# Kernel tuning notes

Measured on AMD Instinct MI355X. Metric: run time of the kernel, lower is better.

The kernel has to match this reference:

```python
import jax, jax.numpy as jnp
import numpy as np

BN_EPS = 1e-5

def _conv1x1(w, b, x):
    # w: (O, C), b: (O,), x: (B, C, T) -> (B, O, T)
    return jnp.einsum('oc,bct->bot', w, x) + b[None, :, None]

def _maxpool2(x):
    # MaxPool1d(kernel_size=2, stride=2): (B, C, T) -> (B, C, T//2)
    B, C, T = x.shape
    return x.reshape(B, C, T // 2, 2).max(axis=-1)

def setup_inputs() -> dict:
    key = jax.random.key(0)
    ks = jax.random.split(key, 11)
    B, C, Ci, T = 4, 256, 128, 8192
    s_in = 1.0 / np.sqrt(C)
    s_ic = 1.0 / np.sqrt(Ci)
    return {
        'x':       jax.random.normal(ks[0], (B, C, T), dtype=jnp.float32),
        'theta_w': jax.random.uniform(ks[1], (Ci, C), jnp.float32, -s_in, s_in),
        'theta_b': jax.random.uniform(ks[2], (Ci,),   jnp.float32, -s_in, s_in),
        'phi_w':   jax.random.uniform(ks[3], (Ci, C), jnp.float32, -s_in, s_in),
        'phi_b':   jax.random.uniform(ks[4], (Ci,),   jnp.float32, -s_in, s_in),
        'g_w':     jax.random.uniform(ks[5], (Ci, C), jnp.float32, -s_in, s_in),
        'g_b':     jax.random.uniform(ks[6], (Ci,),   jnp.float32, -s_in, s_in),
        'w_w':     jax.random.uniform(ks[7], (C, Ci), jnp.float32, -s_ic, s_ic),
        'w_b':     jax.random.uniform(ks[8], (C,),    jnp.float32, -s_ic, s_ic),
        'gamma':   jax.random.normal(ks[9], (C,), dtype=jnp.float32),
        'beta':    jax.random.normal(ks[10], (C,), dtype=jnp.float32),
    }

def reference(x, theta_w, theta_b, phi_w, phi_b, g_w, g_b, w_w, w_b, gamma, beta):
    # x: (B, C, T)
    theta = _conv1x1(theta_w, theta_b, x)            # (B, Ci, T)
    phi   = _maxpool2(_conv1x1(phi_w, phi_b, x))     # (B, Ci, N), N = T//2
    g     = _maxpool2(_conv1x1(g_w, g_b, x))         # (B, Ci, N)
    N = phi.shape[-1]
    # f = theta^T phi / N  (dot-product similarity, divide-by-N normalization)
    f = jnp.einsum('bct,bcn->btn', theta, phi) / N   # (B, T, N)
    y = jnp.einsum('btn,bcn->bct', f, g)             # (B, Ci, T)
    wy = _conv1x1(w_w, w_b, y)                       # (B, C, T)
    # BatchNorm1d (training mode: batch statistics over (B, T), biased var)
    mean = wy.mean(axis=(0, 2), keepdims=True)
    var = ((wy - mean) ** 2).mean(axis=(0, 2), keepdims=True)
    bn = gamma[None, :, None] * (wy - mean) * jax.lax.rsqrt(var + BN_EPS) + beta[None, :, None]
    return bn + x
```

## Files before the change

kernel.cpp:

```cpp
#include <hip/hip_runtime.h>
#include <hip/hip_bf16.h>


constexpr int B = 4, C = 256, CI = 128, T = 8192, NN = 4096;
constexpr int KP = 768, BK = 32, NSTEP = KP / BK;

using s16x8 = __attribute__((ext_vector_type(8))) short;
using f32x4 = __attribute__((ext_vector_type(4))) float;

__device__ __forceinline__ unsigned short f2bf(float f) {
    unsigned int x = __float_as_uint(f);
    unsigned int r = (x + 0x7fffu + ((x >> 16) & 1u)) >> 16;
    return (unsigned short)r;
}
__device__ __forceinline__ float bf2f(unsigned short u) {
    return __uint_as_float((unsigned int)u << 16);
}

#define MFMA(a, b, c) __builtin_amdgcn_mfma_f32_16x16x32_bf16((a), (b), (c), 0, 0, 0)

__device__ __forceinline__ void glds16(const unsigned short* g, void* l) {
    __builtin_amdgcn_global_load_lds(
        (const __attribute__((address_space(1))) unsigned int*)(g),
        (__attribute__((address_space(3))) unsigned int*)(l), 16, 0, 0);
}

constexpr size_t SZ_XT = (size_t)B * T * C * 2;
constexpr size_t O_XTH = 0;
constexpr size_t O_XTL = O_XTH + SZ_XT;
constexpr size_t O_WSH = O_XTL + SZ_XT;
constexpr size_t O_WSL = O_WSH + (size_t)C * C * 2;
constexpr size_t SZ_P  = (size_t)B * CI * NN * 2;
constexpr size_t O_PH  = O_WSL + (size_t)C * C * 2;
constexpr size_t O_PL  = O_PH + SZ_P;
constexpr size_t O_GH  = O_PL + SZ_P;
constexpr size_t O_GL  = O_GH + SZ_P;
constexpr size_t O_S   = O_GL + SZ_P;
constexpr size_t O_M   = O_S  + (size_t)B * CI * CI * 4;
constexpr size_t O_W2H = O_M  + (size_t)B * C * CI * 4;
constexpr size_t O_W2L = O_W2H + (size_t)B * C * C * 2;
constexpr size_t O_B2  = O_W2L + (size_t)B * C * C * 2;
constexpr size_t O_GS  = O_B2 + (size_t)B * C * 4;
constexpr size_t O_GQ  = O_GS + (size_t)C * 4;
constexpr size_t O_A   = O_GQ + (size_t)C * 4;
constexpr size_t O_SH  = O_A  + (size_t)C * 4;

__global__ __launch_bounds__(256) void k0_split(
    const float* __restrict__ x, unsigned short* __restrict__ xth,
    unsigned short* __restrict__ xtl)
{
    __shared__ float xs[64][65];
    int t0 = blockIdx.x * 64, c0 = blockIdx.y * 64, b = blockIdx.z;
    int tid = threadIdx.x;
    const float* xb = x + (size_t)b * C * T;
    #pragma unroll
    for (int p = 0; p < 4; ++p) {
        int idx = tid + p * 256;
        int cr = idx >> 4;
        int tg = (idx & 15) * 4;
        float4 v = *reinterpret_cast<const float4*>(xb + (size_t)(c0 + cr) * T + t0 + tg);
        xs[tg + 0][cr] = v.x; xs[tg + 1][cr] = v.y;
        xs[tg + 2][cr] = v.z; xs[tg + 3][cr] = v.w;
    }
    __syncthreads();
    #pragma unroll
    for (int p = 0; p < 2; ++p) {
        int idx = tid + p * 256;
        int cg = idx & 7, tl = idx >> 3;
        s16x8 hs, ls;
        #pragma unroll
        for (int j = 0; j < 8; ++j) {
            float v = xs[tl][cg * 8 + j];
            unsigned short h = f2bf(v);
            unsigned short l = f2bf(v - bf2f(h));
            hs[j] = (short)h; ls[j] = (short)l;
        }
        size_t dst = ((size_t)b * T + t0 + tl) * C + c0 + cg * 8;
        *reinterpret_cast<s16x8*>(xth + dst) = hs;
        *reinterpret_cast<s16x8*>(xtl + dst) = ls;
    }
}

__global__ __launch_bounds__(256) void k0w(
    const float* __restrict__ phi_w, const float* __restrict__ g_w,
    unsigned short* __restrict__ wsh, unsigned short* __restrict__ wsl)
{
    int idx = blockIdx.x * 256 + threadIdx.x;
    int row = idx >> 8, c = idx & 255;
    float v = (row < CI) ? phi_w[(size_t)row * C + c] : g_w[(size_t)(row - CI) * C + c];
    unsigned short h = f2bf(v);
    wsh[idx] = h;
    wsl[idx] = f2bf(v - bf2f(h));
}

#define STAGE_(buf, kk) {                                                      \
    const int r_ = (kk) >> 8, cb_ = (kk) & 255;                                \
    const unsigned short* As_ = (r_ == 1) ? aSrcL : aSrcH;                     \
    const unsigned short* Bs_ = (r_ == 2) ? bSrcL : bSrcH;                     \
    const unsigned short* ga_ = As_ + (size_t)lane * C + cb_ + w * 8;          \
    const unsigned short* gb_ = Bs_ + (size_t)lane * C + cb_ + w * 8;          \
    char* la_ = arena + ((buf) * 8 + w) * 2048;                                \
    char* lb_ = arena + ((buf) * 8 + 4 + w) * 2048;                            \
    glds16(ga_, la_);                                                          \
    glds16(ga_ + 64 * C, la_ + 1024);                                          \
    glds16(gb_, lb_);                                                          \
    glds16(gb_ + 64 * C, lb_ + 1024);                                          \
}

#define GEMM_LOOP() {                                                          \
    STAGE_(0, 0);                                                              \
    __syncthreads();                                                           \
    int cur = 0;                                                               \
    for (int ks = 0; ks < NSTEP; ++ks) {                                       \
        if (ks + 1 < NSTEP) { STAGE_(cur ^ 1, (ks + 1) * BK); }                \
        s16x8 af[4], bf[4];                                                    \
        _Pragma("unroll")                                                      \
        for (int ts = 0; ts < 4; ++ts)                                         \
            af[ts] = *(const s16x8*)(arena + (cur * 8 + lk) * 2048             \
                                     + (wt * 64 + ts * 16 + lr) * 16);         \
        _Pragma("unroll")                                                      \
        for (int os = 0; os < 4; ++os)                                         \
            bf[os] = *(const s16x8*)(arena + (cur * 8 + 4 + lk) * 2048         \
                                     + (wo * 64 + os * 16 + lr) * 16);         \
        _Pragma("unroll")                                                      \
        for (int os = 0; os < 4; ++os)                                         \
            _Pragma("unroll")                                                  \
            for (int ts = 0; ts < 4; ++ts)                                     \
                acc[os][ts] = MFMA(af[ts], bf[os], acc[os][ts]);               \
        __syncthreads();                                                       \
        cur ^= 1;                                                              \
    }                                                                          \
}

__global__ __launch_bounds__(256) void k1_mfma(
    const unsigned short* __restrict__ xth, const unsigned short* __restrict__ xtl,
    const unsigned short* __restrict__ wsh, const unsigned short* __restrict__ wsl,
    const float* __restrict__ phi_b, const float* __restrict__ g_b,
    unsigned short* __restrict__ ph, unsigned short* __restrict__ pl,
    unsigned short* __restrict__ gh, unsigned short* __restrict__ gl)
{
    const int b = blockIdx.z, t0 = blockIdx.x * 128, isG = blockIdx.y;
    __shared__ __align__(16) char arena[33280];
    const int tid = threadIdx.x, lane = tid & 63, w = tid >> 6;
    const int lr = lane & 15, lk = lane >> 4;
    const int wt = w >> 1, wo = w & 1;

    const unsigned short* aSrcH = xth + (size_t)(b * T + t0) * C;
    const unsigned short* aSrcL = xtl + (size_t)(b * T + t0) * C;
    const unsigned short* bSrcH = wsh + (size_t)(isG * CI) * C;
    const unsigned short* bSrcL = wsl + (size_t)(isG * CI) * C;

    f32x4 acc[4][4];
    #pragma unroll
    for (int i = 0; i < 4; ++i)
        #pragma unroll
        for (int j = 0; j < 4; ++j) acc[i][j] = (f32x4){0.f, 0.f, 0.f, 0.f};

    GEMM_LOOP()

    unsigned int (*pool_s)[65] = (unsigned int (*)[65])arena;
    const float* biasArr = isG ? g_b : phi_b;
    #pragma unroll
    for (int os = 0; os < 4; ++os) {
        int oL = wo * 64 + os * 16 + lr;
        float bias = biasArr[oL];
        #pragma unroll
        for (int ts = 0; ts < 4; ++ts) {
            f32x4 v = acc[os][ts];
            float m0 = fmaxf(v[0], v[1]) + bias;
            float m1 = fmaxf(v[2], v[3]) + bias;
            int nl = wt * 32 + ts * 8 + lk * 2;
            unsigned short h0 = f2bf(m0), h1 = f2bf(m1);
            pool_s[oL][nl]     = (unsigned int)h0 | ((unsigned int)f2bf(m0 - bf2f(h0)) << 16);
            pool_s[oL][nl + 1] = (unsigned int)h1 | ((unsigned int)f2bf(m1 - bf2f(h1)) << 16);
        }
    }
    __syncthreads();
    int oL = tid >> 1, seg = tid & 1;
    size_t n0 = (size_t)(t0 >> 1) + seg * 32;
    unsigned short* dh = (isG ? gh : ph) + ((size_t)b * CI + oL) * NN + n0;
    unsigned short* dl = (isG ? gl : pl) + ((size_t)b * CI + oL) * NN + n0;
    #pragma unroll
    for (int g4 = 0; g4 < 4; ++g4) {
        s16x8 hs, ls;
        #pragma unroll
        for (int j = 0; j < 8; ++j) {
            unsigned int u = pool_s[oL][seg * 32 + g4 * 8 + j];
            hs[j] = (short)(u & 0xffffu);
            ls[j] = (short)(u >> 16);
        }
        *reinterpret_cast<s16x8*>(dh + g4 * 8) = hs;
        *reinterpret_cast<s16x8*>(dl + g4 * 8) = ls;
    }
}

template <int MODE>
__global__ __launch_bounds__(256) void k45_mfma(
    const unsigned short* __restrict__ xth, const unsigned short* __restrict__ xtl,
    const unsigned short* __restrict__ w2h, const unsigned short* __restrict__ w2l,
    const float* __restrict__ b2, const float* __restrict__ x,
    const float* __restrict__ abuf, const float* __restrict__ shbuf,
    float* __restrict__ gsum, float* __restrict__ gsq, float* __restrict__ out)
{
    const int b = blockIdx.z, t0 = blockIdx.x * 128, o0 = blockIdx.y * 128;
    __shared__ __align__(16) char arena[32768];
    const int tid = threadIdx.x, lane = tid & 63, w = tid >> 6;
    const int lr = lane & 15, lk = lane >> 4;
    const int wt = w >> 1, wo = w & 1;

    const unsigned short* aSrcH = xth + (size_t)(b * T + t0) * C;
    const unsigned short* aSrcL = xtl + (size_t)(b * T + t0) * C;
    const unsigned short* bSrcH = w2h + ((size_t)b * C + o0) * C;
    const unsigned short* bSrcL = w2l + ((size_t)b * C + o0) * C;

    f32x4 acc[4][4];
    #pragma unroll
    for (int i = 0; i < 4; ++i)
        #pragma unroll
        for (int j = 0; j < 4; ++j) acc[i][j] = (f32x4){0.f, 0.f, 0.f, 0.f};

    GEMM_LOOP()

    #pragma unroll
    for (int os = 0; os < 4; ++os) {
        int o = o0 + wo * 64 + os * 16 + lr;
        float bv = b2[(size_t)b * C + o];
        if (MODE == 0) {
            float s = 0.f, q = 0.f;
            #pragma unroll
            for (int ts = 0; ts < 4; ++ts)
                #pragma unroll
                for (int r = 0; r < 4; ++r) {
                    float v = acc[os][ts][r] + bv;
                    s += v; q += v * v;
                }
            s += __shfl_xor(s, 16); s += __shfl_xor(s, 32);
            q += __shfl_xor(q, 16); q += __shfl_xor(q, 32);
            if (lk == 0) { atomicAdd(&gsum[o], s); atomicAdd(&gsq[o], q); }
        } else {
            float av = abuf[o], sv = shbuf[o];
            #pragma unroll
            for (int ts = 0; ts < 4; ++ts) {
                int t = t0 + wt * 64 + ts * 16 + lk * 4;
                size_t base = ((size_t)b * C + o) * T + t;
                float4 xv = *reinterpret_cast<const float4*>(x + base);
                float4 ov;
                ov.x = av * (acc[os][ts][0] + bv) + sv + xv.x;
                ov.y = av * (acc[os][ts][1] + bv) + sv + xv.y;
                ov.z = av * (acc[os][ts][2] + bv) + sv + xv.z;
                ov.w = av * (acc[os][ts][3] + bv) + sv + xv.w;
                *reinterpret_cast<float4*>(out + base) = ov;
            }
        }
    }
}

__global__ __launch_bounds__(256) void k2_mfma(
    const unsigned short* __restrict__ ph, const unsigned short* __restrict__ pl,
    const unsigned short* __restrict__ gh, const unsigned short* __restrict__ gl,
    float* __restrict__ S)
{
    int b = blockIdx.y, n0 = blockIdx.x * 128;
    int tid = threadIdx.x, lane = tid & 63, w = tid >> 6;
    int lr = lane & 15, lk = lane >> 4;

    f32x4 acc[2][8];
    #pragma unroll
    for (int i = 0; i < 2; ++i)
        #pragma unroll
        for (int j = 0; j < 8; ++j) acc[i][j] = (f32x4){0.f, 0.f, 0.f, 0.f};

    const unsigned short* ah_b = gh + ((size_t)b * CI + w * 32 + lr) * NN + n0 + lk * 8;
    const unsigned short* al_b = gl + ((size_t)b * CI + w * 32 + lr) * NN + n0 + lk * 8;
    const unsigned short* bh_b = ph + ((size_t)b * CI + lr) * NN + n0 + lk * 8;
    const unsigned short* bl_b = pl + ((size_t)b * CI + lr) * NN + n0 + lk * 8;

    for (int ks = 0; ks < 4; ++ks) {
        s16x8 Ah[2], Al[2], Bh[8], Bl[8];
        #pragma unroll
        for (int is = 0; is < 2; ++is) {
            Ah[is] = *reinterpret_cast<const s16x8*>(ah_b + (size_t)is * 16 * NN + ks * 32);
            Al[is] = *reinterpret_cast<const s16x8*>(al_b + (size_t)is * 16 * NN + ks * 32);
        }
        #pragma unroll
        for (int js = 0; js < 8; ++js) {
            Bh[js] = *reinterpret_cast<const s16x8*>(bh_b + (size_t)js * 16 * NN + ks * 32);
            Bl[js] = *reinterpret_cast<const s16x8*>(bl_b + (size_t)js * 16 * NN + ks * 32);
        }
        #pragma unroll
        for (int is = 0; is < 2; ++is)
            #pragma unroll
            for (int js = 0; js < 8; ++js) {
                acc[is][js] = MFMA(Ah[is], Bh[js], acc[is][js]);
                acc[is][js] = MFMA(Al[is], Bh[js], acc[is][js]);
                acc[is][js] = MFMA(Ah[is], Bl[js], acc[is][js]);
            }
    }
    #pragma unroll
    for (int is = 0; is < 2; ++is) {
        int i0 = w * 32 + is * 16 + lk * 4;
        #pragma unroll
        for (int js = 0; js < 8; ++js) {
            int j = js * 16 + lr;
            #pragma unroll
            for (int r = 0; r < 4; ++r)
                atomicAdd(&S[((size_t)b * CI + i0 + r) * CI + j], acc[is][js][r]);
        }
    }
}

__global__ __launch_bounds__(256) void k3a_M(
    const float* __restrict__ w_w, const float* __restrict__ S, float* __restrict__ M)
{
    int idx = blockIdx.x * 256 + threadIdx.x;
    int j4 = (idx & 31) * 4;
    int r  = (idx >> 5) & (C - 1);
    int b  = idx >> 13;
    const float* Sb = S + (size_t)b * CI * CI;
    const float* wr = w_w + (size_t)r * CI;
    float4 a = {0.f, 0.f, 0.f, 0.f};
    for (int k = 0; k < CI; ++k) {
        float wv = wr[k];
        float4 s = *reinterpret_cast<const float4*>(&Sb[(size_t)k * CI + j4]);
        a.x += wv * s.x; a.y += wv * s.y; a.z += wv * s.z; a.w += wv * s.w;
    }
    const float sc = 1.f / NN;
    a.x *= sc; a.y *= sc; a.z *= sc; a.w *= sc;
    *reinterpret_cast<float4*>(&M[((size_t)b * C + r) * CI + j4]) = a;
}

__global__ __launch_bounds__(256) void k3b_W2(
    const float* __restrict__ M, const float* __restrict__ theta_w,
    const float* __restrict__ theta_b, const float* __restrict__ w_b,
    unsigned short* __restrict__ w2h, unsigned short* __restrict__ w2l,
    float* __restrict__ b2)
{
    int idx = blockIdx.x * 256 + threadIdx.x;
    int c4 = (idx & 63) * 4;
    int r  = (idx >> 6) & (C - 1);
    int b  = idx >> 14;
    const float* Mb = M + ((size_t)b * C + r) * CI;
    float4 a = {0.f, 0.f, 0.f, 0.f};
    for (int k = 0; k < CI; ++k) {
        float mv = Mb[k];
        float4 tw = *reinterpret_cast<const float4*>(&theta_w[(size_t)k * C + c4]);
        a.x += mv * tw.x; a.y += mv * tw.y; a.z += mv * tw.z; a.w += mv * tw.w;
    }
    size_t ob = ((size_t)b * C + r) * C + c4;
    float av[4] = {a.x, a.y, a.z, a.w};
    #pragma unroll
    for (int i = 0; i < 4; ++i) {
        unsigned short h = f2bf(av[i]);
        w2h[ob + i] = h;
        w2l[ob + i] = f2bf(av[i] - bf2f(h));
    }
    if (c4 == 0) {
        float bv = 0.f;
        for (int k = 0; k < CI; ++k) bv += Mb[k] * theta_b[k];
        b2[(size_t)b * C + r] = bv + w_b[r];
    }
}

__global__ void k4b_stats(const float* __restrict__ gsum, const float* __restrict__ gsq,
                          const float* __restrict__ gamma, const float* __restrict__ beta,
                          float* __restrict__ a, float* __restrict__ sh)
{
    int c = threadIdx.x;
    const float invBT = 1.f / (float)(B * T);
    float mean = gsum[c] * invBT;
    float var  = gsq[c] * invBT - mean * mean;
    float av = gamma[c] * rsqrtf(var + 1e-5f);
    a[c]  = av;
    sh[c] = beta[c] - av * mean;
}

extern "C" void kernel_launch(void* const* d_in, const int* in_sizes, int n_in,
                              void* d_out, int out_size, void* d_ws, size_t ws_size,
                              hipStream_t stream)
{
    const float* x       = (const float*)d_in[0];
    const float* theta_w = (const float*)d_in[1];
    const float* theta_b = (const float*)d_in[2];
    const float* phi_w   = (const float*)d_in[3];
    const float* phi_b   = (const float*)d_in[4];
    const float* g_w     = (const float*)d_in[5];
    const float* g_b     = (const float*)d_in[6];
    const float* w_w     = (const float*)d_in[7];
    const float* w_b     = (const float*)d_in[8];
    const float* gamma   = (const float*)d_in[9];
    const float* beta    = (const float*)d_in[10];
    float* out = (float*)d_out;
    char* ws = (char*)d_ws;

    unsigned short* xth = (unsigned short*)(ws + O_XTH);
    unsigned short* xtl = (unsigned short*)(ws + O_XTL);
    unsigned short* wsh = (unsigned short*)(ws + O_WSH);
    unsigned short* wsl = (unsigned short*)(ws + O_WSL);
    unsigned short* ph  = (unsigned short*)(ws + O_PH);
    unsigned short* pl  = (unsigned short*)(ws + O_PL);
    unsigned short* gh  = (unsigned short*)(ws + O_GH);
    unsigned short* gl  = (unsigned short*)(ws + O_GL);
    float* Sbuf  = (float*)(ws + O_S);
    float* Mbuf  = (float*)(ws + O_M);
    unsigned short* w2h = (unsigned short*)(ws + O_W2H);
    unsigned short* w2l = (unsigned short*)(ws + O_W2L);
    float* b2    = (float*)(ws + O_B2);
    float* gsum  = (float*)(ws + O_GS);
    float* gsq   = (float*)(ws + O_GQ);
    float* abuf  = (float*)(ws + O_A);
    float* shbuf = (float*)(ws + O_SH);

    hipMemsetAsync(Sbuf, 0, (size_t)B * CI * CI * sizeof(float), stream);
    hipMemsetAsync(gsum, 0, 2 * (size_t)C * sizeof(float), stream);

    k0_split<<<dim3(T / 64, C / 64, B), 256, 0, stream>>>(x, xth, xtl);
    k0w<<<dim3(C * C / 256), 256, 0, stream>>>(phi_w, g_w, wsh, wsl);
    k1_mfma<<<dim3(T / 128, 2, B), 256, 0, stream>>>(xth, xtl, wsh, wsl, phi_b, g_b,
                                                     ph, pl, gh, gl);
    k2_mfma<<<dim3(NN / 128, B), 256, 0, stream>>>(ph, pl, gh, gl, Sbuf);
    k3a_M<<<dim3(B * C * CI / 4 / 256), 256, 0, stream>>>(w_w, Sbuf, Mbuf);
    k3b_W2<<<dim3(B * C * C / 4 / 256), 256, 0, stream>>>(Mbuf, theta_w, theta_b, w_b,
                                                          w2h, w2l, b2);
    k45_mfma<0><<<dim3(T / 128, C / 128, B), 256, 0, stream>>>(
        xth, xtl, w2h, w2l, b2, x, abuf, shbuf, gsum, gsq, out);
    k4b_stats<<<1, C, 0, stream>>>(gsum, gsq, gamma, beta, abuf, shbuf);
    k45_mfma<1><<<dim3(T / 128, C / 128, B), 256, 0, stream>>>(
        xth, xtl, w2h, w2l, b2, x, abuf, shbuf, gsum, gsq, out);
}
```

Before: 249.6 us.

## Store operands pre-tiled and stream GEMM B operand directly from global

The bf16 hi/lo split of x and both weight matrices are now written in a tiled layout: 128-row tiles with 8-element K-chunks placed contiguously. The GEMM kernels load a whole 128x256 A tile into 64KB of LDS in one shot and read the B fragments straight from global memory. The old double-buffered 24-step K loop with a barrier per step becomes three phases (hi*hi, hi*lo, lo*hi) separated by only a few barriers. In exchange, LDS use doubles, which can lower occupancy, and the B loads are no longer staged through LDS, so their global-memory latency sits inside the MFMA loop.

```diff
diff --git a/kernel.cpp b/kernel.cpp
--- a/kernel.cpp
+++ b/kernel.cpp
@@ -3,7 +3,6 @@
 
 
 constexpr int B = 4, C = 256, CI = 128, T = 8192, NN = 4096;
-constexpr int KP = 768, BK = 32, NSTEP = KP / BK;
 
 using s16x8 = __attribute__((ext_vector_type(8))) short;
 using f32x4 = __attribute__((ext_vector_type(4))) float;
@@ -24,6 +23,7 @@
         (const __attribute__((address_space(1))) unsigned int*)(g),
         (__attribute__((address_space(3))) unsigned int*)(l), 16, 0, 0);
 }
+
 
 constexpr size_t SZ_XT = (size_t)B * T * C * 2;
 constexpr size_t O_XTH = 0;
@@ -63,19 +63,22 @@
         xs[tg + 2][cr] = v.z; xs[tg + 3][cr] = v.w;
     }
     __syncthreads();
+    size_t tileBase = ((size_t)b * (T / 128) + (t0 >> 7)) * 32768;
+    int trBase = t0 & 127;
     #pragma unroll
     for (int p = 0; p < 2; ++p) {
         int idx = tid + p * 256;
-        int cg = idx & 7, tl = idx >> 3;
+        int kcL = idx >> 6;
+        int tl  = idx & 63;
         s16x8 hs, ls;
         #pragma unroll
         for (int j = 0; j < 8; ++j) {
-            float v = xs[tl][cg * 8 + j];
+            float v = xs[tl][kcL * 8 + j];
             unsigned short h = f2bf(v);
             unsigned short l = f2bf(v - bf2f(h));
             hs[j] = (short)h; ls[j] = (short)l;
         }
-        size_t dst = ((size_t)b * T + t0 + tl) * C + c0 + cg * 8;
+        size_t dst = tileBase + (size_t)((c0 >> 3) + kcL) * 1024 + (trBase + tl) * 8;
         *reinterpret_cast<s16x8*>(xth + dst) = hs;
         *reinterpret_cast<s16x8*>(xtl + dst) = ls;
     }
@@ -86,50 +89,57 @@
     unsigned short* __restrict__ wsh, unsigned short* __restrict__ wsl)
 {
     int idx = blockIdx.x * 256 + threadIdx.x;
-    int row = idx >> 8, c = idx & 255;
-    float v = (row < CI) ? phi_w[(size_t)row * C + c] : g_w[(size_t)(row - CI) * C + c];
-    unsigned short h = f2bf(v);
-    wsh[idx] = h;
-    wsl[idx] = f2bf(v - bf2f(h));
-}
-
-#define STAGE_(buf, kk) {                                                      \
-    const int r_ = (kk) >> 8, cb_ = (kk) & 255;                                \
-    const unsigned short* As_ = (r_ == 1) ? aSrcL : aSrcH;                     \
-    const unsigned short* Bs_ = (r_ == 2) ? bSrcL : bSrcH;                     \
-    const unsigned short* ga_ = As_ + (size_t)lane * C + cb_ + w * 8;          \
-    const unsigned short* gb_ = Bs_ + (size_t)lane * C + cb_ + w * 8;          \
-    char* la_ = arena + ((buf) * 8 + w) * 2048;                                \
-    char* lb_ = arena + ((buf) * 8 + 4 + w) * 2048;                            \
-    glds16(ga_, la_);                                                          \
-    glds16(ga_ + 64 * C, la_ + 1024);                                          \
-    glds16(gb_, lb_);                                                          \
-    glds16(gb_ + 64 * C, lb_ + 1024);                                          \
-}
-
-#define GEMM_LOOP() {                                                          \
-    STAGE_(0, 0);                                                              \
+    int c8 = idx & 31, row = idx >> 5;
+    const float* src = (row < CI) ? &phi_w[(size_t)row * C + c8 * 8]
+                                  : &g_w[(size_t)(row - CI) * C + c8 * 8];
+    s16x8 hs, ls;
+    #pragma unroll
+    for (int j = 0; j < 8; ++j) {
+        float v = src[j];
+        unsigned short h = f2bf(v);
+        hs[j] = (short)h; ls[j] = (short)f2bf(v - bf2f(h));
+    }
+    size_t dst = (size_t)(row >> 7) * 32768 + (size_t)c8 * 1024 + (row & 127) * 8;
+    *reinterpret_cast<s16x8*>(wsh + dst) = hs;
+    *reinterpret_cast<s16x8*>(wsl + dst) = ls;
+}
+
+#define STAGE_A(srcT) {                                                        \
+    _Pragma("unroll")                                                          \
+    for (int i_ = 0; i_ < 16; ++i_)                                            \
+        glds16((srcT) + (size_t)(w * 8192 + i_ * 512 + lane * 8),              \
+               arena + w * 16384 + i_ * 1024);                                 \
+}
+
+#define K8(BT) {                                                               \
+    _Pragma("unroll")                                                          \
+    for (int ks_ = 0; ks_ < 8; ++ks_) {                                        \
+        s16x8 af[4], bfr[4];                                                   \
+        _Pragma("unroll")                                                      \
+        for (int ts_ = 0; ts_ < 4; ++ts_)                                      \
+            af[ts_] = *(const s16x8*)(arena + (ks_ * 4 + lk) * 2048            \
+                                      + (wt * 64 + ts_ * 16 + lr) * 16);       \
+        _Pragma("unroll")                                                      \
+        for (int os_ = 0; os_ < 4; ++os_)                                      \
+            bfr[os_] = *(const s16x8*)((BT) + (size_t)(ks_ * 4 + lk) * 1024    \
+                                       + (wo * 64 + os_ * 16 + lr) * 8);       \
+        _Pragma("unroll")                                                      \
+        for (int os_ = 0; os_ < 4; ++os_)                                      \
+            _Pragma("unroll")                                                  \
+            for (int ts_ = 0; ts_ < 4; ++ts_)                                  \
+                acc[os_][ts_] = MFMA(af[ts_], bfr[os_], acc[os_][ts_]);        \
+    }                                                                          \
+}
+
+#define GEMM_3PHASE(aT_h, aT_l, bT_h, bT_l) {                                  \
+    STAGE_A(aT_h);                                                             \
     __syncthreads();                                                           \
-    int cur = 0;                                                               \
-    for (int ks = 0; ks < NSTEP; ++ks) {                                       \
-        if (ks + 1 < NSTEP) { STAGE_(cur ^ 1, (ks + 1) * BK); }                \
-        s16x8 af[4], bf[4];                                                    \
-        _Pragma("unroll")                                                      \
-        for (int ts = 0; ts < 4; ++ts)                                         \
-            af[ts] = *(const s16x8*)(arena + (cur * 8 + lk) * 2048             \
-                                     + (wt * 64 + ts * 16 + lr) * 16);         \
-        _Pragma("unroll")                                                      \
-        for (int os = 0; os < 4; ++os)                                         \
-            bf[os] = *(const s16x8*)(arena + (cur * 8 + 4 + lk) * 2048         \
-                                     + (wo * 64 + os * 16 + lr) * 16);         \
-        _Pragma("unroll")                                                      \
-        for (int os = 0; os < 4; ++os)                                         \
-            _Pragma("unroll")                                                  \
-            for (int ts = 0; ts < 4; ++ts)                                     \
-                acc[os][ts] = MFMA(af[ts], bf[os], acc[os][ts]);               \
-        __syncthreads();                                                       \
-        cur ^= 1;                                                              \
-    }                                                                          \
+    K8(bT_h);                                                                  \
+    K8(bT_l);                                                                  \
+    __syncthreads();                                                           \
+    STAGE_A(aT_l);                                                             \
+    __syncthreads();                                                           \
+    K8(bT_h);                                                                  \
 }
 
 __global__ __launch_bounds__(256) void k1_mfma(
@@ -140,15 +150,15 @@
     unsigned short* __restrict__ gh, unsigned short* __restrict__ gl)
 {
     const int b = blockIdx.z, t0 = blockIdx.x * 128, isG = blockIdx.y;
-    __shared__ __align__(16) char arena[33280];
+    __shared__ __align__(16) char arena[65536];
     const int tid = threadIdx.x, lane = tid & 63, w = tid >> 6;
     const int lr = lane & 15, lk = lane >> 4;
     const int wt = w >> 1, wo = w & 1;
 
-    const unsigned short* aSrcH = xth + (size_t)(b * T + t0) * C;
-    const unsigned short* aSrcL = xtl + (size_t)(b * T + t0) * C;
-    const unsigned short* bSrcH = wsh + (size_t)(isG * CI) * C;
-    const unsigned short* bSrcL = wsl + (size_t)(isG * CI) * C;
+    const unsigned short* aTh = xth + ((size_t)b * (T / 128) + (t0 >> 7)) * 32768;
+    const unsigned short* aTl = xtl + ((size_t)b * (T / 128) + (t0 >> 7)) * 32768;
+    const unsigned short* bTh = wsh + (size_t)isG * 32768;
+    const unsigned short* bTl = wsl + (size_t)isG * 32768;
 
     f32x4 acc[4][4];
     #pragma unroll
@@ -156,7 +166,8 @@
         #pragma unroll
         for (int j = 0; j < 4; ++j) acc[i][j] = (f32x4){0.f, 0.f, 0.f, 0.f};
 
-    GEMM_LOOP()
+    GEMM_3PHASE(aTh, aTl, bTh, bTl)
+    __syncthreads();
 
     unsigned int (*pool_s)[65] = (unsigned int (*)[65])arena;
     const float* biasArr = isG ? g_b : phi_b;
@@ -202,16 +213,17 @@
     const float* __restrict__ abuf, const float* __restrict__ shbuf,
     float* __restrict__ gsum, float* __restrict__ gsq, float* __restrict__ out)
 {
-    const int b = blockIdx.z, t0 = blockIdx.x * 128, o0 = blockIdx.y * 128;
-    __shared__ __align__(16) char arena[32768];
+    const int b = blockIdx.z, t0 = blockIdx.x * 128, oHalf = blockIdx.y;
+    const int o0 = oHalf * 128;
+    __shared__ __align__(16) char arena[65536];
     const int tid = threadIdx.x, lane = tid & 63, w = tid >> 6;
     const int lr = lane & 15, lk = lane >> 4;
     const int wt = w >> 1, wo = w & 1;
 
-    const unsigned short* aSrcH = xth + (size_t)(b * T + t0) * C;
-    const unsigned short* aSrcL = xtl + (size_t)(b * T + t0) * C;
-    const unsigned short* bSrcH = w2h + ((size_t)b * C + o0) * C;
-    const unsigned short* bSrcL = w2l + ((size_t)b * C + o0) * C;
+    const unsigned short* aTh = xth + ((size_t)b * (T / 128) + (t0 >> 7)) * 32768;
+    const unsigned short* aTl = xtl + ((size_t)b * (T / 128) + (t0 >> 7)) * 32768;
+    const unsigned short* bTh = w2h + ((size_t)b * 2 + oHalf) * 32768;
+    const unsigned short* bTl = w2l + ((size_t)b * 2 + oHalf) * 32768;
 
     f32x4 acc[4][4];
     #pragma unroll
@@ -219,7 +231,7 @@
         #pragma unroll
         for (int j = 0; j < 4; ++j) acc[i][j] = (f32x4){0.f, 0.f, 0.f, 0.f};
 
-    GEMM_LOOP()
+    GEMM_3PHASE(aTh, aTl, bTh, bTl)
 
     #pragma unroll
     for (int os = 0; os < 4; ++os) {
@@ -336,25 +348,30 @@
     float* __restrict__ b2)
 {
     int idx = blockIdx.x * 256 + threadIdx.x;
-    int c4 = (idx & 63) * 4;
-    int r  = (idx >> 6) & (C - 1);
-    int b  = idx >> 14;
+    int c8 = idx & 31;
+    int r  = (idx >> 5) & (C - 1);
+    int b  = idx >> 13;
     const float* Mb = M + ((size_t)b * C + r) * CI;
-    float4 a = {0.f, 0.f, 0.f, 0.f};
+    float4 a0 = {0.f, 0.f, 0.f, 0.f}, a1 = {0.f, 0.f, 0.f, 0.f};
     for (int k = 0; k < CI; ++k) {
         float mv = Mb[k];
-        float4 tw = *reinterpret_cast<const float4*>(&theta_w[(size_t)k * C + c4]);
-        a.x += mv * tw.x; a.y += mv * tw.y; a.z += mv * tw.z; a.w += mv * tw.w;
-    }
-    size_t ob = ((size_t)b * C + r) * C + c4;
-    float av[4] = {a.x, a.y, a.z, a.w};
-    #pragma unroll
-    for (int i = 0; i < 4; ++i) {
+        const float* tw = &theta_w[(size_t)k * C + c8 * 8];
+        float4 t0 = *reinterpret_cast<const float4*>(tw);
+        float4 t1 = *reinterpret_cast<const float4*>(tw + 4);
+        a0.x += mv * t0.x; a0.y += mv * t0.y; a0.z += mv * t0.z; a0.w += mv * t0.w;
+        a1.x += mv * t1.x; a1.y += mv * t1.y; a1.z += mv * t1.z; a1.w += mv * t1.w;
+    }
+    float av[8] = {a0.x, a0.y, a0.z, a0.w, a1.x, a1.y, a1.z, a1.w};
+    s16x8 hs, ls;
+    #pragma unroll
+    for (int i = 0; i < 8; ++i) {
         unsigned short h = f2bf(av[i]);
-        w2h[ob + i] = h;
-        w2l[ob + i] = f2bf(av[i] - bf2f(h));
-    }
-    if (c4 == 0) {
+        hs[i] = (short)h; ls[i] = (short)f2bf(av[i] - bf2f(h));
+    }
+    size_t dst = ((size_t)b * 2 + (r >> 7)) * 32768 + (size_t)c8 * 1024 + (r & 127) * 8;
+    *reinterpret_cast<s16x8*>(w2h + dst) = hs;
+    *reinterpret_cast<s16x8*>(w2l + dst) = ls;
+    if (c8 == 0) {
         float bv = 0.f;
         for (int k = 0; k < CI; ++k) bv += Mb[k] * theta_b[k];
         b2[(size_t)b * C + r] = bv + w_b[r];
@@ -414,12 +431,12 @@
     hipMemsetAsync(gsum, 0, 2 * (size_t)C * sizeof(float), stream);
 
     k0_split<<<dim3(T / 64, C / 64, B), 256, 0, stream>>>(x, xth, xtl);
-    k0w<<<dim3(C * C / 256), 256, 0, stream>>>(phi_w, g_w, wsh, wsl);
+    k0w<<<dim3(32), 256, 0, stream>>>(phi_w, g_w, wsh, wsl);
     k1_mfma<<<dim3(T / 128, 2, B), 256, 0, stream>>>(xth, xtl, wsh, wsl, phi_b, g_b,
                                                      ph, pl, gh, gl);
     k2_mfma<<<dim3(NN / 128, B), 256, 0, stream>>>(ph, pl, gh, gl, Sbuf);
     k3a_M<<<dim3(B * C * CI / 4 / 256), 256, 0, stream>>>(w_w, Sbuf, Mbuf);
-    k3b_W2<<<dim3(B * C * C / 4 / 256), 256, 0, stream>>>(Mbuf, theta_w, theta_b, w_b,
+    k3b_W2<<<dim3(B * C * C / 8 / 256), 256, 0, stream>>>(Mbuf, theta_w, theta_b, w_b,
                                                           w2h, w2l, b2);
     k45_mfma<0><<<dim3(T / 128, C / 128, B), 256, 0, stream>>>(
         xth, xtl, w2h, w2l, b2, x, abuf, shbuf, gsum, gsq, out);
```

Measured after the change: 253.4 us. No clear change (+1.5%).
